# Optimization experiments

Measured on AMD Instinct MI355X. Metric: run time of the kernel, lower is better.

Reference implementation:

```python
import jax, jax.numpy as jnp
import numpy as np

K = 8  # number of nearest neighbors


def knn_graph(x, k):
    """Binary k-NN adjacency: A[i, j] = 1 iff j is among the k nearest
    neighbors of i (self excluded), matching torch cdist + topk + scatter."""
    n = x.shape[0]
    sq = jnp.sum(x * x, axis=1)  # [n]
    # Squared euclidean distances (same ordering as cdist for top-k).
    d = sq[:, None] + sq[None, :] - 2.0 * (x @ x.T)  # [n, n]
    # Exclude self by pushing the diagonal to +inf.
    d = d + jnp.where(jnp.eye(n, dtype=bool), jnp.inf, 0.0).astype(x.dtype)
    _, idx = jax.lax.top_k(-d, k)  # k smallest distances -> [n, k]
    rows = jnp.arange(n)[:, None]  # [n, 1]
    a = jnp.zeros((n, n), dtype=x.dtype).at[rows, idx].set(1.0)
    return a


def bce_mean(p, t):
    """F.binary_cross_entropy with reduction='mean'; torch clamps log at -100."""
    log_p = jnp.clip(jnp.log(p), -100.0)
    log_1mp = jnp.clip(jnp.log1p(-p), -100.0)
    return jnp.mean(-(t * log_p + (1.0 - t) * log_1mp))


def setup_inputs() -> dict:
    key = jax.random.key(0)
    kx, kz = jax.random.split(key)
    X = jax.random.normal(kx, (8192, 128), dtype=jnp.float32)
    Z = jax.random.normal(kz, (8192, 32), dtype=jnp.float32)
    return {"X": X, "Z": Z}


def reference(X, Z):
    A_X = knn_graph(X, K)
    A_Z = knn_graph(Z, K)
    return bce_mean(A_Z, A_X)
```

## Files before the change

kernel.cpp:

```cpp
#include <hip/hip_runtime.h>
#include <hip/hip_bf16.h>
#include <math.h>

#define N_PTS 8192
#define KNN 8
#define JSPLIT 32
#define WAVES 4
#define NQ 4
#define QT_PER_BLOCK (WAVES * NQ)
#define JCHUNK (N_PTS / JSPLIT)
#define JTILES (JCHUNK / 16)
#define NTILE (N_PTS / 16)
#define NBX (NTILE / QT_PER_BLOCK)
#define NPART (NBX * JSPLIT)

typedef __attribute__((ext_vector_type(8))) short bf16x8;
typedef __attribute__((ext_vector_type(4))) float f32x4;

__device__ __forceinline__ float med3(float a, float b, float c) {
    return __builtin_amdgcn_fmed3f(a, b, c);
}

__device__ __forceinline__ void insertv(float v, float (&d)[8]) {
    float p = d[0];
    d[0] = fminf(v, d[0]);
#pragma unroll
    for (int k = 1; k < 8; ++k) {
        float q = d[k];
        d[k] = med3(v, p, q);
        p = q;
    }
}

template <int D>
__global__ __launch_bounds__(256) void prep_sq(const float* __restrict__ x,
                                               float* __restrict__ sq) {
    const int row = (blockIdx.x * 256 + threadIdx.x) >> 6;
    const int lane = threadIdx.x & 63;
    float s = 0.f;
    if constexpr (D == 128) {
        float2 v = *reinterpret_cast<const float2*>(x + (size_t)row * D + lane * 2);
        s = fmaf(v.x, v.x, v.y * v.y);
    } else {
        float v = (lane < D) ? x[(size_t)row * D + lane] : 0.f;
        s = v * v;
    }
#pragma unroll
    for (int o = 32; o > 0; o >>= 1) s += __shfl_down(s, o);
    if (lane == 0) sq[row] = s;
}

template <int D>
__global__ __launch_bounds__(256) void pack_kernel(const float* __restrict__ x,
                                                   bf16x8* __restrict__ pk) {
    constexpr int KB = D / 32;
    const int gid = blockIdx.x * 256 + threadIdx.x;
    const int l = gid & 63;
    const int kb = (gid >> 6) % KB;
    const int tile = gid / (64 * KB);
    const float* src = x + (size_t)(tile * 16 + (l & 15)) * D + kb * 32 + (l >> 4) * 8;
    bf16x8 v;
#pragma unroll
    for (int e = 0; e < 8; ++e) {
        __hip_bfloat16 h = __float2bfloat16(src[e]);
        v[e] = *reinterpret_cast<short*>(&h);
    }
    pk[gid] = v;
}

template <int D>
__global__ __launch_bounds__(256, 3) void thresh_scan(const bf16x8* __restrict__ pk,
                                                      const float* __restrict__ sq,
                                                      float* __restrict__ pd) {
    constexpr int KB = D / 32;
    const int lane = threadIdx.x & 63;
    const int w = __builtin_amdgcn_readfirstlane((int)(threadIdx.x >> 6));
    const int qt0 = blockIdx.x * QT_PER_BLOCK + w * NQ;
    const int js = blockIdx.y;
    const int t0 = js * JTILES;
    const int lrow = lane & 15;
    const int jr = (lane >> 4) * 4;

    bf16x8 bfrag[NQ][KB];
#pragma unroll
    for (int q = 0; q < NQ; ++q)
#pragma unroll
        for (int kb = 0; kb < KB; ++kb)
            bfrag[q][kb] = pk[((size_t)(qt0 + q) * KB + kb) * 64 + lane];

    float d8[NQ][8];
#pragma unroll
    for (int q = 0; q < NQ; ++q)
#pragma unroll
        for (int k = 0; k < 8; ++k) d8[q][k] = __builtin_inff();

#pragma unroll 2
    for (int tt = t0; tt < t0 + JTILES; ++tt) {
        bf16x8 af[KB];
#pragma unroll
        for (int kb = 0; kb < KB; ++kb) af[kb] = pk[((size_t)tt * KB + kb) * 64 + lane];
        f32x4 acc[NQ];
#pragma unroll
        for (int q = 0; q < NQ; ++q) acc[q] = (f32x4){0.f, 0.f, 0.f, 0.f};
#pragma unroll
        for (int kb = 0; kb < KB; ++kb)
#pragma unroll
            for (int q = 0; q < NQ; ++q)
                acc[q] = __builtin_amdgcn_mfma_f32_16x16x32_bf16(af[kb], bfrag[q][kb], acc[q], 0, 0, 0);

        f32x4 sq4 = *reinterpret_cast<const f32x4*>(sq + tt * 16 + jr);
#pragma unroll
        for (int q = 0; q < NQ; ++q) {
            if (tt == qt0 + q) {
#pragma unroll
                for (int r = 0; r < 4; ++r) {
                    float dist = fmaf(-2.f, acc[q][r], sq4[r]);
                    if (jr + r == lrow) dist = __builtin_inff();
                    insertv(dist, d8[q]);
                }
            } else {
#pragma unroll
                for (int r = 0; r < 4; ++r) insertv(fmaf(-2.f, acc[q][r], sq4[r]), d8[q]);
            }
        }
    }

    __shared__ float lds_d[WAVES][NQ][64][8];
#pragma unroll
    for (int q = 0; q < NQ; ++q)
#pragma unroll
        for (int k = 0; k < 8; ++k) lds_d[w][q][lane][k] = d8[q][k];
    __syncthreads();
    {
        const int t = threadIdx.x;
        const int bq = t >> 4;
        const int col = t & 15;
        const int w2 = bq >> 2;
        const int q2 = bq & 3;
        float e[8];
#pragma unroll
        for (int k = 0; k < 8; ++k) e[k] = lds_d[w2][q2][col][k];
#pragma unroll
        for (int p = 1; p < 4; ++p)
#pragma unroll
            for (int k = 0; k < 8; ++k) insertv(lds_d[w2][q2][p * 16 + col][k], e);
        const int row = (blockIdx.x * QT_PER_BLOCK + bq) * 16 + col;
        const size_t o = ((size_t)js * N_PTS + row) * 8;
#pragma unroll
        for (int k = 0; k < 8; ++k) pd[o + k] = e[k];
    }
}

__global__ __launch_bounds__(256) void thresh_merge(const float* __restrict__ pd,
                                                    float* __restrict__ t) {
    const int row = blockIdx.x * 256 + threadIdx.x;
    float d8[8];
#pragma unroll
    for (int k = 0; k < 8; ++k) d8[k] = __builtin_inff();
    for (int js = 0; js < JSPLIT; ++js) {
        const f32x4* p = reinterpret_cast<const f32x4*>(pd + ((size_t)js * N_PTS + row) * 8);
        f32x4 a = p[0], b = p[1];
        insertv(a[0], d8); insertv(a[1], d8); insertv(a[2], d8); insertv(a[3], d8);
        insertv(b[0], d8); insertv(b[1], d8); insertv(b[2], d8); insertv(b[3], d8);
    }
    t[row] = d8[7];
}

__global__ __launch_bounds__(256, 3) void count_scan(const bf16x8* __restrict__ pkX,
                                                     const float* __restrict__ sqX,
                                                     const float* __restrict__ tX,
                                                     const bf16x8* __restrict__ pkZ,
                                                     const float* __restrict__ sqZ,
                                                     const float* __restrict__ tZ,
                                                     int* __restrict__ partial) {
    const int lane = threadIdx.x & 63;
    const int w = __builtin_amdgcn_readfirstlane((int)(threadIdx.x >> 6));
    const int qt0 = blockIdx.x * QT_PER_BLOCK + w * NQ;
    const int js = blockIdx.y;
    const int t0 = js * JTILES;
    const int lrow = lane & 15;
    const int jr = (lane >> 4) * 4;

    bf16x8 bfX[NQ][4];
    bf16x8 bfZ[NQ];
    float tx[NQ], tz[NQ];
#pragma unroll
    for (int q = 0; q < NQ; ++q) {
#pragma unroll
        for (int kb = 0; kb < 4; ++kb) bfX[q][kb] = pkX[((size_t)(qt0 + q) * 4 + kb) * 64 + lane];
        bfZ[q] = pkZ[(size_t)(qt0 + q) * 64 + lane];
        tx[q] = tX[(qt0 + q) * 16 + lrow];
        tz[q] = tZ[(qt0 + q) * 16 + lrow];
    }

    int c = 0;
#pragma unroll 2
    for (int tt = t0; tt < t0 + JTILES; ++tt) {
        bf16x8 afX[4];
#pragma unroll
        for (int kb = 0; kb < 4; ++kb) afX[kb] = pkX[((size_t)tt * 4 + kb) * 64 + lane];
        bf16x8 afZ = pkZ[(size_t)tt * 64 + lane];

        f32x4 accX[NQ], accZ[NQ];
#pragma unroll
        for (int q = 0; q < NQ; ++q) {
            accX[q] = (f32x4){0.f, 0.f, 0.f, 0.f};
            accZ[q] = (f32x4){0.f, 0.f, 0.f, 0.f};
        }
#pragma unroll
        for (int kb = 0; kb < 4; ++kb)
#pragma unroll
            for (int q = 0; q < NQ; ++q)
                accX[q] = __builtin_amdgcn_mfma_f32_16x16x32_bf16(afX[kb], bfX[q][kb], accX[q], 0, 0, 0);
#pragma unroll
        for (int q = 0; q < NQ; ++q)
            accZ[q] = __builtin_amdgcn_mfma_f32_16x16x32_bf16(afZ, bfZ[q], accZ[q], 0, 0, 0);

        f32x4 sx4 = *reinterpret_cast<const f32x4*>(sqX + tt * 16 + jr);
        f32x4 sz4 = *reinterpret_cast<const f32x4*>(sqZ + tt * 16 + jr);
#pragma unroll
        for (int q = 0; q < NQ; ++q) {
            if (tt == qt0 + q) {
#pragma unroll
                for (int r = 0; r < 4; ++r) {
                    float dx = fmaf(-2.f, accX[q][r], sx4[r]);
                    float dz = fmaf(-2.f, accZ[q][r], sz4[r]);
                    c += (dx <= tx[q] && dz <= tz[q] && (jr + r != lrow)) ? 1 : 0;
                }
            } else {
#pragma unroll
                for (int r = 0; r < 4; ++r) {
                    float dx = fmaf(-2.f, accX[q][r], sx4[r]);
                    float dz = fmaf(-2.f, accZ[q][r], sz4[r]);
                    c += (dx <= tx[q] && dz <= tz[q]) ? 1 : 0;
                }
            }
        }
    }

#pragma unroll
    for (int o = 32; o > 0; o >>= 1) c += __shfl_down(c, o);
    __shared__ int wsum[WAVES];
    if (lane == 0) wsum[w] = c;
    __syncthreads();
    if (threadIdx.x == 0)
        partial[blockIdx.y * NBX + blockIdx.x] = wsum[0] + wsum[1] + wsum[2] + wsum[3];
}

__global__ void finalize_kernel(const int* __restrict__ partial, float* __restrict__ out) {
    int v = 0;
    for (int k = threadIdx.x; k < NPART; k += 256) v += partial[k];
#pragma unroll
    for (int o = 32; o > 0; o >>= 1) v += __shfl_down(v, o);
    __shared__ int wsum[4];
    if ((threadIdx.x & 63) == 0) wsum[threadIdx.x >> 6] = v;
    __syncthreads();
    if (threadIdx.x == 0) {
        double m = (double)(wsum[0] + wsum[1] + wsum[2] + wsum[3]);
        out[0] = (float)((2.0 * KNN * N_PTS - 2.0 * m) * 100.0 / ((double)N_PTS * (double)N_PTS));
    }
}

extern "C" void kernel_launch(void* const* d_in, const int* in_sizes, int n_in,
                              void* d_out, int out_size, void* d_ws, size_t ws_size,
                              hipStream_t stream) {
    const float* X = (const float*)d_in[0];
    const float* Z = (const float*)d_in[1];
    float* out = (float*)d_out;
    char* ws = (char*)d_ws;

    bf16x8* pkX = (bf16x8*)(ws);
    bf16x8* pkZ = (bf16x8*)(ws + 2097152);
    float* sqX = (float*)(ws + 2621440);
    float* sqZ = (float*)(ws + 2654208);
    float* pdX = (float*)(ws + 2686976);
    float* pdZ = (float*)(ws + 11075584);
    float* tX = (float*)(ws + 19464192);
    float* tZ = (float*)(ws + 19496960);
    int* partial = (int*)(ws + 19529728);

    prep_sq<128><<<N_PTS / 4, 256, 0, stream>>>(X, sqX);
    prep_sq<32><<<N_PTS / 4, 256, 0, stream>>>(Z, sqZ);
    pack_kernel<128><<<NTILE * 4 * 64 / 256, 256, 0, stream>>>(X, pkX);
    pack_kernel<32><<<NTILE * 1 * 64 / 256, 256, 0, stream>>>(Z, pkZ);
    thresh_scan<128><<<dim3(NBX, JSPLIT), 256, 0, stream>>>(pkX, sqX, pdX);
    thresh_scan<32><<<dim3(NBX, JSPLIT), 256, 0, stream>>>(pkZ, sqZ, pdZ);
    thresh_merge<<<N_PTS / 256, 256, 0, stream>>>(pdX, tX);
    thresh_merge<<<N_PTS / 256, 256, 0, stream>>>(pdZ, tZ);
    count_scan<<<dim3(NBX, JSPLIT), 256, 0, stream>>>(pkX, sqX, tX, pkZ, sqZ, tZ, partial);
    finalize_kernel<<<1, 256, 0, stream>>>(partial, out);
}
```

Baseline: 185.8 us.

## Stage column tiles through double-buffered LDS shared by all waves

```diff
diff --git a/kernel.cpp b/kernel.cpp
--- a/kernel.cpp
+++ b/kernel.cpp
@@ -4,14 +4,16 @@
 
 #define N_PTS 8192
 #define KNN 8
-#define JSPLIT 32
+#define JSPLIT 16
 #define WAVES 4
-#define NQ 4
+#define NQ 2
 #define QT_PER_BLOCK (WAVES * NQ)
+#define NTILE (N_PTS / 16)
+#define NBX (NTILE / QT_PER_BLOCK)
 #define JCHUNK (N_PTS / JSPLIT)
 #define JTILES (JCHUNK / 16)
-#define NTILE (N_PTS / 16)
-#define NBX (NTILE / QT_PER_BLOCK)
+#define TB 2
+#define NB (JTILES / TB)
 #define NPART (NBX * JSPLIT)
 
 typedef __attribute__((ext_vector_type(8))) short bf16x8;
@@ -69,12 +71,17 @@
 }
 
 template <int D>
-__global__ __launch_bounds__(256, 3) void thresh_scan(const bf16x8* __restrict__ pk,
+__global__ __launch_bounds__(256, 4) void thresh_scan(const bf16x8* __restrict__ pk,
                                                       const float* __restrict__ sq,
                                                       float* __restrict__ pd) {
     constexpr int KB = D / 32;
-    const int lane = threadIdx.x & 63;
-    const int w = __builtin_amdgcn_readfirstlane((int)(threadIdx.x >> 6));
+    constexpr int BCH = TB * KB * 64;
+    __shared__ bf16x8 sbuf[2][BCH];
+    __shared__ float lds_d[WAVES][NQ][64][8];
+
+    const int t = threadIdx.x;
+    const int lane = t & 63;
+    const int w = __builtin_amdgcn_readfirstlane(t >> 6);
     const int qt0 = blockIdx.x * QT_PER_BLOCK + w * NQ;
     const int js = blockIdx.y;
     const int t0 = js * JTILES;
@@ -94,49 +101,80 @@
 #pragma unroll
         for (int k = 0; k < 8; ++k) d8[q][k] = __builtin_inff();
 
-#pragma unroll 2
-    for (int tt = t0; tt < t0 + JTILES; ++tt) {
-        bf16x8 af[KB];
-#pragma unroll
-        for (int kb = 0; kb < KB; ++kb) af[kb] = pk[((size_t)tt * KB + kb) * 64 + lane];
-        f32x4 acc[NQ];
-#pragma unroll
-        for (int q = 0; q < NQ; ++q) acc[q] = (f32x4){0.f, 0.f, 0.f, 0.f};
-#pragma unroll
-        for (int kb = 0; kb < KB; ++kb)
-#pragma unroll
-            for (int q = 0; q < NQ; ++q)
-                acc[q] = __builtin_amdgcn_mfma_f32_16x16x32_bf16(af[kb], bfrag[q][kb], acc[q], 0, 0, 0);
-
-        f32x4 sq4 = *reinterpret_cast<const f32x4*>(sq + tt * 16 + jr);
-#pragma unroll
-        for (int q = 0; q < NQ; ++q) {
-            if (tt == qt0 + q) {
-#pragma unroll
-                for (int r = 0; r < 4; ++r) {
-                    float dist = fmaf(-2.f, acc[q][r], sq4[r]);
-                    if (jr + r == lrow) dist = __builtin_inff();
-                    insertv(dist, d8[q]);
+    {
+        const size_t gb = (size_t)t0 * KB * 64;
+        if constexpr (BCH == 512) {
+            sbuf[0][t] = pk[gb + t];
+            sbuf[0][t + 256] = pk[gb + t + 256];
+        } else {
+            if (t < BCH) sbuf[0][t] = pk[gb + t];
+        }
+    }
+    __syncthreads();
+
+    int cur = 0;
+    bf16x8 stg0, stg1;
+    for (int b = 0; b < NB; ++b) {
+        if (b + 1 < NB) {
+            const size_t gb = (size_t)(t0 + (b + 1) * TB) * KB * 64;
+            if constexpr (BCH == 512) {
+                stg0 = pk[gb + t];
+                stg1 = pk[gb + t + 256];
+            } else {
+                if (t < BCH) stg0 = pk[gb + t];
+            }
+        }
+#pragma unroll
+        for (int u = 0; u < TB; ++u) {
+            const int tt = t0 + b * TB + u;
+            f32x4 acc[NQ];
+#pragma unroll
+            for (int q = 0; q < NQ; ++q) acc[q] = (f32x4){0.f, 0.f, 0.f, 0.f};
+#pragma unroll
+            for (int kb = 0; kb < KB; ++kb) {
+                bf16x8 af = sbuf[cur][u * KB * 64 + kb * 64 + lane];
+#pragma unroll
+                for (int q = 0; q < NQ; ++q)
+                    acc[q] = __builtin_amdgcn_mfma_f32_16x16x32_bf16(af, bfrag[q][kb], acc[q], 0, 0, 0);
+            }
+            f32x4 sq4 = *reinterpret_cast<const f32x4*>(sq + tt * 16 + jr);
+#pragma unroll
+            for (int q = 0; q < NQ; ++q) {
+                if (tt == qt0 + q) {
+#pragma unroll
+                    for (int r = 0; r < 4; ++r) {
+                        float dist = fmaf(-2.f, acc[q][r], sq4[r]);
+                        if (jr + r == lrow) dist = __builtin_inff();
+                        insertv(dist, d8[q]);
+                    }
+                } else {
+#pragma unroll
+                    for (int r = 0; r < 4; ++r) insertv(fmaf(-2.f, acc[q][r], sq4[r]), d8[q]);
                 }
+            }
+        }
+        if (b + 1 < NB) {
+            if constexpr (BCH == 512) {
+                sbuf[cur ^ 1][t] = stg0;
+                sbuf[cur ^ 1][t + 256] = stg1;
             } else {
-#pragma unroll
-                for (int r = 0; r < 4; ++r) insertv(fmaf(-2.f, acc[q][r], sq4[r]), d8[q]);
-            }
-        }
-    }
-
-    __shared__ float lds_d[WAVES][NQ][64][8];
+                if (t < BCH) sbuf[cur ^ 1][t] = stg0;
+            }
+        }
+        __syncthreads();
+        cur ^= 1;
+    }
+
 #pragma unroll
     for (int q = 0; q < NQ; ++q)
 #pragma unroll
         for (int k = 0; k < 8; ++k) lds_d[w][q][lane][k] = d8[q][k];
     __syncthreads();
-    {
-        const int t = threadIdx.x;
+    if (t < QT_PER_BLOCK * 16) {
         const int bq = t >> 4;
         const int col = t & 15;
-        const int w2 = bq >> 2;
-        const int q2 = bq & 3;
+        const int w2 = bq >> 1;
+        const int q2 = bq & 1;
         float e[8];
 #pragma unroll
         for (int k = 0; k < 8; ++k) e[k] = lds_d[w2][q2][col][k];
@@ -166,15 +204,20 @@
     t[row] = d8[7];
 }
 
-__global__ __launch_bounds__(256, 3) void count_scan(const bf16x8* __restrict__ pkX,
+__global__ __launch_bounds__(256, 4) void count_scan(const bf16x8* __restrict__ pkX,
                                                      const float* __restrict__ sqX,
                                                      const float* __restrict__ tX,
                                                      const bf16x8* __restrict__ pkZ,
                                                      const float* __restrict__ sqZ,
                                                      const float* __restrict__ tZ,
                                                      int* __restrict__ partial) {
-    const int lane = threadIdx.x & 63;
-    const int w = __builtin_amdgcn_readfirstlane((int)(threadIdx.x >> 6));
+    __shared__ bf16x8 sbX[2][TB * 4 * 64];
+    __shared__ bf16x8 sbZ[2][TB * 1 * 64];
+    __shared__ int wsum[WAVES];
+
+    const int t = threadIdx.x;
+    const int lane = t & 63;
+    const int w = __builtin_amdgcn_readfirstlane(t >> 6);
     const int qt0 = blockIdx.x * QT_PER_BLOCK + w * NQ;
     const int js = blockIdx.y;
     const int t0 = js * JTILES;
@@ -193,57 +236,83 @@
         tz[q] = tZ[(qt0 + q) * 16 + lrow];
     }
 
+    {
+        const size_t gx = (size_t)t0 * 4 * 64;
+        const size_t gz = (size_t)t0 * 64;
+        sbX[0][t] = pkX[gx + t];
+        sbX[0][t + 256] = pkX[gx + t + 256];
+        if (t < TB * 64) sbZ[0][t] = pkZ[gz + t];
+    }
+    __syncthreads();
+
     int c = 0;
-#pragma unroll 2
-    for (int tt = t0; tt < t0 + JTILES; ++tt) {
-        bf16x8 afX[4];
-#pragma unroll
-        for (int kb = 0; kb < 4; ++kb) afX[kb] = pkX[((size_t)tt * 4 + kb) * 64 + lane];
-        bf16x8 afZ = pkZ[(size_t)tt * 64 + lane];
-
-        f32x4 accX[NQ], accZ[NQ];
-#pragma unroll
-        for (int q = 0; q < NQ; ++q) {
-            accX[q] = (f32x4){0.f, 0.f, 0.f, 0.f};
-            accZ[q] = (f32x4){0.f, 0.f, 0.f, 0.f};
-        }
-#pragma unroll
-        for (int kb = 0; kb < 4; ++kb)
-#pragma unroll
-            for (int q = 0; q < NQ; ++q)
-                accX[q] = __builtin_amdgcn_mfma_f32_16x16x32_bf16(afX[kb], bfX[q][kb], accX[q], 0, 0, 0);
-#pragma unroll
-        for (int q = 0; q < NQ; ++q)
-            accZ[q] = __builtin_amdgcn_mfma_f32_16x16x32_bf16(afZ, bfZ[q], accZ[q], 0, 0, 0);
-
-        f32x4 sx4 = *reinterpret_cast<const f32x4*>(sqX + tt * 16 + jr);
-        f32x4 sz4 = *reinterpret_cast<const f32x4*>(sqZ + tt * 16 + jr);
-#pragma unroll
-        for (int q = 0; q < NQ; ++q) {
-            if (tt == qt0 + q) {
-#pragma unroll
-                for (int r = 0; r < 4; ++r) {
-                    float dx = fmaf(-2.f, accX[q][r], sx4[r]);
-                    float dz = fmaf(-2.f, accZ[q][r], sz4[r]);
-                    c += (dx <= tx[q] && dz <= tz[q] && (jr + r != lrow)) ? 1 : 0;
+    int cur = 0;
+    bf16x8 sx0, sx1, sz0;
+    for (int b = 0; b < NB; ++b) {
+        if (b + 1 < NB) {
+            const size_t gx = (size_t)(t0 + (b + 1) * TB) * 4 * 64;
+            const size_t gz = (size_t)(t0 + (b + 1) * TB) * 64;
+            sx0 = pkX[gx + t];
+            sx1 = pkX[gx + t + 256];
+            if (t < TB * 64) sz0 = pkZ[gz + t];
+        }
+#pragma unroll
+        for (int u = 0; u < TB; ++u) {
+            const int tt = t0 + b * TB + u;
+            f32x4 accX[NQ], accZ[NQ];
+#pragma unroll
+            for (int q = 0; q < NQ; ++q) {
+                accX[q] = (f32x4){0.f, 0.f, 0.f, 0.f};
+                accZ[q] = (f32x4){0.f, 0.f, 0.f, 0.f};
+            }
+#pragma unroll
+            for (int kb = 0; kb < 4; ++kb) {
+                bf16x8 af = sbX[cur][u * 4 * 64 + kb * 64 + lane];
+#pragma unroll
+                for (int q = 0; q < NQ; ++q)
+                    accX[q] = __builtin_amdgcn_mfma_f32_16x16x32_bf16(af, bfX[q][kb], accX[q], 0, 0, 0);
+            }
+            {
+                bf16x8 afZ = sbZ[cur][u * 64 + lane];
+#pragma unroll
+                for (int q = 0; q < NQ; ++q)
+                    accZ[q] = __builtin_amdgcn_mfma_f32_16x16x32_bf16(afZ, bfZ[q], accZ[q], 0, 0, 0);
+            }
+            f32x4 sx4 = *reinterpret_cast<const f32x4*>(sqX + tt * 16 + jr);
+            f32x4 sz4 = *reinterpret_cast<const f32x4*>(sqZ + tt * 16 + jr);
+#pragma unroll
+            for (int q = 0; q < NQ; ++q) {
+                if (tt == qt0 + q) {
+#pragma unroll
+                    for (int r = 0; r < 4; ++r) {
+                        float dx = fmaf(-2.f, accX[q][r], sx4[r]);
+                        float dz = fmaf(-2.f, accZ[q][r], sz4[r]);
+                        c += (dx <= tx[q] && dz <= tz[q] && (jr + r != lrow)) ? 1 : 0;
+                    }
+                } else {
+#pragma unroll
+                    for (int r = 0; r < 4; ++r) {
+                        float dx = fmaf(-2.f, accX[q][r], sx4[r]);
+                        float dz = fmaf(-2.f, accZ[q][r], sz4[r]);
+                        c += (dx <= tx[q] && dz <= tz[q]) ? 1 : 0;
+                    }
                 }
-            } else {
-#pragma unroll
-                for (int r = 0; r < 4; ++r) {
-                    float dx = fmaf(-2.f, accX[q][r], sx4[r]);
-                    float dz = fmaf(-2.f, accZ[q][r], sz4[r]);
-                    c += (dx <= tx[q] && dz <= tz[q]) ? 1 : 0;
-                }
-            }
-        }
+            }
+        }
+        if (b + 1 < NB) {
+            sbX[cur ^ 1][t] = sx0;
+            sbX[cur ^ 1][t + 256] = sx1;
+            if (t < TB * 64) sbZ[cur ^ 1][t] = sz0;
+        }
+        __syncthreads();
+        cur ^= 1;
     }
 
 #pragma unroll
     for (int o = 32; o > 0; o >>= 1) c += __shfl_down(c, o);
-    __shared__ int wsum[WAVES];
     if (lane == 0) wsum[w] = c;
     __syncthreads();
-    if (threadIdx.x == 0)
+    if (t == 0)
         partial[blockIdx.y * NBX + blockIdx.x] = wsum[0] + wsum[1] + wsum[2] + wsum[3];
 }
 
```

Result: faster. 167.4 us (-9.9%).
